# Performance work log

Measured on AMD Instinct MI355X. Metric: run time of the kernel, lower is better.

Reference implementation:

```python
import jax, jax.numpy as jnp
import numpy as np

B, N, D = 8, 1024, 768
H = 12
HD = D // H  # 64
SCALE = HD ** -0.5


def setup_inputs() -> dict:
    key = jax.random.key(0)
    k1, k2, k3 = jax.random.split(key, 3)
    x = jax.random.normal(k1, (B, N, D), dtype=jnp.float32)
    qkv_w = jax.random.normal(k2, (3 * D, D), dtype=jnp.float32) * 0.02
    proj_w = jax.random.normal(k3, (D, D), dtype=jnp.float32) * 0.02
    proj_b = jnp.zeros((D,), dtype=jnp.float32)
    return {"x": x, "qkv_w": qkv_w, "proj_w": proj_w, "proj_b": proj_b}


def reference(x, qkv_w, proj_w, proj_b):
    # qkv projection: [B,N,3D] -> [3,B,H,N,HD]
    qkv = jnp.einsum('bnd,ed->bne', x, qkv_w)
    qkv = qkv.reshape(B, N, 3, H, HD).transpose(2, 0, 3, 1, 4)
    q, k, v = qkv[0], qkv[1], qkv[2]
    # scaled dot-product attention
    attn = jnp.einsum('bhqd,bhkd->bhqk', q * SCALE, k)
    attn = jax.nn.softmax(attn, axis=-1)
    out = jnp.einsum('bhqk,bhkd->bhqd', attn, v)
    out = out.transpose(0, 2, 1, 3).reshape(B, N, D)
    # output projection
    return jnp.einsum('bnd,ed->bne', out, proj_w) + proj_b
```

## Files before the change

### kernel.cpp

```cpp
#include <hip/hip_runtime.h>

typedef unsigned short ushort;
typedef __attribute__((ext_vector_type(4)))  float  f32x4;
typedef __attribute__((ext_vector_type(16))) float  f32x16;
typedef __attribute__((ext_vector_type(8)))  short  s16x8;
typedef __attribute__((ext_vector_type(4)))  ushort u16x4;
typedef __attribute__((ext_vector_type(4)))  unsigned u32x4;

#define MFMA16(a, b, c) __builtin_amdgcn_mfma_f32_16x16x32_bf16((a), (b), (c), 0, 0, 0)
#define MFMA32(a, b, c) __builtin_amdgcn_mfma_f32_32x32x16_bf16((a), (b), (c), 0, 0, 0)

__device__ __forceinline__ ushort f2bf(float f) {
    unsigned u = __builtin_bit_cast(unsigned, f);
    u = (u + 0x7FFF + ((u >> 16) & 1)) >> 16;
    return (ushort)u;
}

__device__ __forceinline__ unsigned cvtpk_bf16(float lo, float hi) {
    unsigned r;
    asm("v_cvt_pk_bf16_f32 %0, %1, %2" : "=v"(r) : "v"(lo), "v"(hi));
    return r;
}
__device__ __forceinline__ void plswap(unsigned& a, unsigned& b) {
    asm volatile("v_permlane32_swap_b32 %0, %1" : "+v"(a), "+v"(b));
}
__device__ __forceinline__ float pairmax(float x) {
    unsigned a = __builtin_bit_cast(unsigned, x), b;
    asm("v_mov_b32 %0, %1" : "=v"(b) : "v"(a));
    plswap(a, b);
    return fmaxf(__builtin_bit_cast(float, a), __builtin_bit_cast(float, b));
}
__device__ __forceinline__ float pairsum(float x) {
    unsigned a = __builtin_bit_cast(unsigned, x), b;
    asm("v_mov_b32 %0, %1" : "=v"(b) : "v"(a));
    plswap(a, b);
    return __builtin_bit_cast(float, a) + __builtin_bit_cast(float, b);
}
__device__ __forceinline__ float fast_exp2(float x) {
    float r;
    asm("v_exp_f32 %0, %1" : "=v"(r) : "v"(x));
    return r;
}

__device__ __forceinline__ void gload_lds16(const ushort* g, ushort* l) {
    __builtin_amdgcn_global_load_lds(
        (const __attribute__((address_space(1))) void*)g,
        (__attribute__((address_space(3))) void*)l, 16, 0, 0);
}

__global__ __launch_bounds__(256) void cvt_all(
    const float* __restrict__ x, const float* __restrict__ wq,
    const float* __restrict__ wp, ushort* __restrict__ out,
    int n4x, int n4q, int n4p)
{
    int i = blockIdx.x * blockDim.x + threadIdx.x;
    const int stride = gridDim.x * blockDim.x;
    const int total = n4x + n4q + n4p;
    for (; i < total; i += stride) {
        float4 v;
        if (i < n4x)            v = ((const float4*)x)[i];
        else if (i < n4x + n4q) v = ((const float4*)wq)[i - n4x];
        else                    v = ((const float4*)wp)[i - n4x - n4q];
        u16x4 o;
        o[0] = f2bf(v.x); o[1] = f2bf(v.y); o[2] = f2bf(v.z); o[3] = f2bf(v.w);
        ((u16x4*)out)[i] = o;
    }
}

__device__ __forceinline__ void gemm128_mainloop(
    const ushort* __restrict__ A, const ushort* __restrict__ B, int K,
    int row0, int col0, ushort* As, ushort* Bs, f32x4 acc[4][4])
{
    const int t  = threadIdx.x;
    const int l  = t & 63;
    const int w  = t >> 6;
    const int lr = l & 15, lg = l >> 4;
    const int wm = w >> 1, wn = w & 1;

#pragma unroll
    for (int m = 0; m < 4; m++)
#pragma unroll
        for (int n = 0; n < 4; n++) acc[m][n] = (f32x4){0.f, 0.f, 0.f, 0.f};

    const int slot = (t & 3) ^ ((t >> 3) & 3);
    const ushort* ga0 = A + (row0 + (t >> 2)) * K + slot * 8;
    const ushort* gb0 = B + (col0 + (t >> 2)) * K + slot * 8;
    const int rowsz = 64 * K;
    ushort* la0 = As + t * 8;
    ushort* lb0 = Bs + t * 8;

    auto STAGE = [&](int kt, int buf) {
        const int k0  = kt * 32;
        const int off = buf * 4096;
        gload_lds16(ga0 + k0,         la0 + off);
        gload_lds16(ga0 + rowsz + k0, la0 + off + 2048);
        gload_lds16(gb0 + k0,         lb0 + off);
        gload_lds16(gb0 + rowsz + k0, lb0 + off + 2048);
    };
    const int sx = (lg ^ ((lr >> 1) & 3)) * 8;
    auto COMPUTE = [&](int buf) {
        const ushort* Ab = As + buf * 4096;
        const ushort* Bb = Bs + buf * 4096;
        s16x8 af[4], bfr[4];
#pragma unroll
        for (int m = 0; m < 4; m++)
            af[m] = *(const s16x8*)&Ab[(wm * 64 + m * 16 + lr) * 32 + sx];
#pragma unroll
        for (int n = 0; n < 4; n++)
            bfr[n] = *(const s16x8*)&Bb[(wn * 64 + n * 16 + lr) * 32 + sx];
        __builtin_amdgcn_s_setprio(1);
#pragma unroll
        for (int m = 0; m < 4; m++)
#pragma unroll
            for (int n = 0; n < 4; n++)
                acc[m][n] = MFMA16(af[m], bfr[n], acc[m][n]);
        __builtin_amdgcn_s_setprio(0);
    };

    const int nt = K >> 5;
    STAGE(0, 0);
    STAGE(1, 1);
    asm volatile("s_waitcnt vmcnt(4)" ::: "memory");
    __builtin_amdgcn_s_barrier();

#define GSTEP(IT, CBUF, SBUF)                                          \
    {                                                                  \
        const int sk = (IT) + 2;                                       \
        const bool st = sk < nt;                                       \
        if (st) STAGE(sk, SBUF);                                       \
        COMPUTE(CBUF);                                                 \
        if (st) { asm volatile("s_waitcnt vmcnt(4)" ::: "memory"); }   \
        else    { asm volatile("s_waitcnt vmcnt(0)" ::: "memory"); }   \
        __builtin_amdgcn_s_barrier();                                  \
    }

    for (int base = 0; base < nt; base += 3) {
        GSTEP(base,     0, 2);
        GSTEP(base + 1, 1, 0);
        GSTEP(base + 2, 2, 1);
    }
#undef GSTEP
}

__global__ __launch_bounds__(256) void qkv_gemm(
    const ushort* __restrict__ X, const ushort* __restrict__ W,
    ushort* __restrict__ qb, ushort* __restrict__ kb, ushort* __restrict__ vb)
{
    __shared__ __align__(16) ushort As[3 * 128 * 32];
    __shared__ __align__(16) ushort Bs[3 * 128 * 32];
    f32x4 acc[4][4];
    const int br = blockIdx.x, bc = blockIdx.y;
    gemm128_mainloop(X, W, 768, br * 128, bc * 128, As, Bs, acc);

    const int t = threadIdx.x, l = t & 63, w = t >> 6;
    const int lr = l & 15, lg = l >> 4, wm = w >> 1, wn = w & 1;
    const int p = (bc * 128) / 768;
    const int mrow0 = br * 128 + wm * 64 + lg * 4;
    const int ecolB = bc * 128 + wn * 64 + lr;
    const float QSCALE = 0.125f * 1.44269504088896f;

#pragma unroll
    for (int n = 0; n < 4; n++) {
        const int e   = ecolB + n * 16;
        const int rem = e - p * 768;
        const int h   = rem >> 6;
        const int hd  = rem & 63;
#pragma unroll
        for (int m = 0; m < 4; m++) {
            const int mr = mrow0 + m * 16;
            const int b  = mr >> 10;
            const int nn = mr & 1023;
            const f32x4 v = acc[m][n];
            const int bh = b * 12 + h;
            if (p == 0) {
                ushort* dst = qb + (bh * 1024 + nn) * 64 + hd;
#pragma unroll
                for (int r = 0; r < 4; r++) dst[r * 64] = f2bf(v[r] * QSCALE);
            } else if (p == 1) {
                ushort* dst = kb + (bh * 1024 + nn) * 64 + hd;
#pragma unroll
                for (int r = 0; r < 4; r++) dst[r * 64] = f2bf(v[r]);
            } else {
                u16x4 pk;
                pk[0] = f2bf(v[0]); pk[1] = f2bf(v[1]);
                pk[2] = f2bf(v[2]); pk[3] = f2bf(v[3]);
                *(u16x4*)(vb + (bh * 64 + hd) * 1024 + nn) = pk;
            }
        }
    }
}

__global__ __launch_bounds__(256) void attn_kernel(
    const ushort* __restrict__ qb, const ushort* __restrict__ kb,
    const ushort* __restrict__ vb, ushort* __restrict__ ao)
{
    __shared__ __align__(16) ushort KV[2][4096];
    const int bh = blockIdx.x, qt = blockIdx.y;
    const int b = bh / 12, h = bh - b * 12;
    const int t = threadIdx.x, l = t & 63, w = t >> 6;
    const int lq = l & 31, hi = l >> 5;
    const int qr0 = qt * 128 + w * 32;

    const int l3 = l >> 3, l7 = l & 7;
    const int ku = w * 8 + l3;
    const int pfv = l7 ^ l3;
    const char* ksrc = (const char*)kb + (size_t)(bh * 1024 + ku) * 128
                     + ((l7 ^ l3) << 4);
    const char* vsrc = (const char*)vb + (size_t)(bh * 64 + ku + 32 * ((pfv >> 2) & 1)) * 2048
                     + ((pfv & 3) << 4);
    ushort* kdst = &KV[0][0]    + w * 512 + l * 8;
    ushort* vdst = &KV[0][2048] + w * 512 + l * 8;

    const ushort* qlane = qb + (bh * 1024 + qr0 + lq) * 64 + hi * 8;
    s16x8 qf[4];
#pragma unroll
    for (int s = 0; s < 4; s++) qf[s] = *(const s16x8*)(qlane + s * 16);

    float m = -__builtin_inff();
    float lsum = 0.f;
    f32x16 o0 = {}, o1 = {};

    gload_lds16((const ushort*)ksrc, kdst);
    gload_lds16((const ushort*)vsrc, vdst);
    __syncthreads();

    const int fx = (lq & 7) << 4;
    for (int it = 0; it < 32; ++it) {
        const int cur = it & 1;
        if (it < 31) {
            const int kvn = (it + 1) * 32;
            gload_lds16((const ushort*)(ksrc + kvn * 128), kdst + (cur ^ 1) * 4096);
            gload_lds16((const ushort*)(vsrc + kvn * 2),   vdst + (cur ^ 1) * 4096);
        }
        const char* Kb = (const char*)&KV[cur][0];
        const char* Vb = (const char*)&KV[cur][2048];

        s16x8 kf[4];
#pragma unroll
        for (int s = 0; s < 4; s++)
            kf[s] = *(const s16x8*)(Kb + lq * 128 + ((hi * 16 + s * 32) ^ fx));

        f32x16 sa = {};
        __builtin_amdgcn_s_setprio(1);
#pragma unroll
        for (int s = 0; s < 4; s++) sa = MFMA32(kf[s], qf[s], sa);
        __builtin_amdgcn_s_setprio(0);

        float g0 = fmaxf(fmaxf(sa[0],  sa[1]),  sa[2]);
        float g1 = fmaxf(fmaxf(sa[3],  sa[4]),  sa[5]);
        float g2 = fmaxf(fmaxf(sa[6],  sa[7]),  sa[8]);
        float g3 = fmaxf(fmaxf(sa[9],  sa[10]), sa[11]);
        float g4 = fmaxf(fmaxf(sa[12], sa[13]), sa[14]);
        float h0 = fmaxf(fmaxf(g0, g1), g2);
        float h1 = fmaxf(fmaxf(g3, g4), sa[15]);
        const float mx = pairmax(fmaxf(h0, h1));

        if (!__all(mx <= m + 8.f)) {
            const float mn = fmaxf(m, mx);
            const float fac = fast_exp2(m - mn);
            m = mn;
            lsum *= fac;
#pragma unroll
            for (int r = 0; r < 16; r++) { o0[r] *= fac; o1[r] *= fac; }
        }

        float p[16];
#pragma unroll
        for (int r = 0; r < 16; r++) p[r] = fast_exp2(sa[r] - m);
        float ts[8];
#pragma unroll
        for (int r = 0; r < 8; r++) ts[r] = p[r] + p[r + 8];
#pragma unroll
        for (int s = 4; s; s >>= 1)
#pragma unroll
            for (int r = 0; r < s; r++) ts[r] += ts[r + s];
        lsum += pairsum(ts[0]);

        s16x8 pfr[2];
#pragma unroll
        for (int slot = 0; slot < 2; slot++) {
            const int r0 = slot * 8;
            unsigned a0 = cvtpk_bf16(p[r0 + 0], p[r0 + 1]);
            unsigned a1 = cvtpk_bf16(p[r0 + 4], p[r0 + 5]);
            plswap(a0, a1);
            unsigned b0 = cvtpk_bf16(p[r0 + 2], p[r0 + 3]);
            unsigned b1 = cvtpk_bf16(p[r0 + 6], p[r0 + 7]);
            plswap(b0, b1);
            const u32x4 u = {a0, b0, a1, b1};
            pfr[slot] = __builtin_bit_cast(s16x8, u);
        }

        s16x8 vf[2][2];
#pragma unroll
        for (int half = 0; half < 2; half++)
#pragma unroll
            for (int s = 0; s < 2; s++)
                vf[half][s] = *(const s16x8*)(Vb + lq * 128 + ((half * 64 + hi * 16 + s * 32) ^ fx));
        __builtin_amdgcn_s_setprio(1);
        o0 = MFMA32(vf[0][0], pfr[0], o0);
        o1 = MFMA32(vf[1][0], pfr[0], o1);
        o0 = MFMA32(vf[0][1], pfr[1], o0);
        o1 = MFMA32(vf[1][1], pfr[1], o1);
        __builtin_amdgcn_s_setprio(0);

        __syncthreads();
    }

    const float inv = 1.f / lsum;
    ushort* op = ao + (b * 1024 + qr0 + lq) * 768 + h * 64 + 4 * hi;
#pragma unroll
    for (int i = 0; i < 4; i++) {
        u16x4 pk0, pk1;
#pragma unroll
        for (int j = 0; j < 4; j++) {
            pk0[j] = f2bf(o0[4 * i + j] * inv);
            pk1[j] = f2bf(o1[4 * i + j] * inv);
        }
        *(u16x4*)(op + 8 * i)      = pk0;
        *(u16x4*)(op + 32 + 8 * i) = pk1;
    }
}

__global__ __launch_bounds__(256) void proj_gemm(
    const ushort* __restrict__ A, const ushort* __restrict__ W,
    const float* __restrict__ bias, float* __restrict__ out)
{
    __shared__ __align__(16) ushort As[3 * 128 * 32];
    __shared__ __align__(16) ushort Bs[3 * 128 * 32];
    f32x4 acc[4][4];
    const int br = blockIdx.x, bc = blockIdx.y;
    gemm128_mainloop(A, W, 768, br * 128, bc * 128, As, Bs, acc);

    const int t = threadIdx.x, l = t & 63, w = t >> 6;
    const int lr = l & 15, lg = l >> 4, wm = w >> 1, wn = w & 1;
    const int mrow0 = br * 128 + wm * 64 + lg * 4;
    const int ecolB = bc * 128 + wn * 64 + lr;

#pragma unroll
    for (int n = 0; n < 4; n++) {
        const int e = ecolB + n * 16;
        const float bv = bias[e];
#pragma unroll
        for (int m = 0; m < 4; m++) {
            const int mr = mrow0 + m * 16;
#pragma unroll
            for (int r = 0; r < 4; r++)
                out[(mr + r) * 768 + e] = acc[m][n][r] + bv;
        }
    }
}

extern "C" void kernel_launch(void* const* d_in, const int* in_sizes, int n_in,
                              void* d_out, int out_size, void* d_ws, size_t ws_size,
                              hipStream_t stream)
{
    const float* x  = (const float*)d_in[0];
    const float* wq = (const float*)d_in[1];
    const float* wp = (const float*)d_in[2];
    const float* pb = (const float*)d_in[3];
    float* out = (float*)d_out;

    const int NX = 8 * 1024 * 768;
    const int NQ = 2304 * 768;
    const int NP = 768 * 768;
    const int SEG = 8 * 12 * 1024 * 64;

    ushort* xb  = (ushort*)d_ws;
    ushort* wqb = xb + NX;
    ushort* wpb = wqb + NQ;
    ushort* qb  = wpb + NP;
    ushort* kb  = qb + SEG;
    ushort* vb  = kb + SEG;
    ushort* ao  = xb;

    cvt_all<<<2048, 256, 0, stream>>>(x, wq, wp, xb, NX / 4, NQ / 4, NP / 4);

    qkv_gemm  <<<dim3(64, 18), 256, 0, stream>>>(xb, wqb, qb, kb, vb);
    attn_kernel<<<dim3(96, 8), 256, 0, stream>>>(qb, kb, vb, ao);
    proj_gemm <<<dim3(64, 6), 256, 0, stream>>>(ao, wpb, pb, out);
}
```

Before: 115.2 us.

## Use 64-key tiles with triple-buffered LDS and MFMA-based row sums in attention

```diff
diff --git a/kernel.cpp b/kernel.cpp
--- a/kernel.cpp
+++ b/kernel.cpp
@@ -29,12 +29,6 @@
     asm("v_mov_b32 %0, %1" : "=v"(b) : "v"(a));
     plswap(a, b);
     return fmaxf(__builtin_bit_cast(float, a), __builtin_bit_cast(float, b));
-}
-__device__ __forceinline__ float pairsum(float x) {
-    unsigned a = __builtin_bit_cast(unsigned, x), b;
-    asm("v_mov_b32 %0, %1" : "=v"(b) : "v"(a));
-    plswap(a, b);
-    return __builtin_bit_cast(float, a) + __builtin_bit_cast(float, b);
 }
 __device__ __forceinline__ float fast_exp2(float x) {
     float r;
@@ -194,119 +188,159 @@
     const ushort* __restrict__ qb, const ushort* __restrict__ kb,
     const ushort* __restrict__ vb, ushort* __restrict__ ao)
 {
-    __shared__ __align__(16) ushort KV[2][4096];
+    __shared__ __align__(16) ushort KV[3][8192];
     const int bh = blockIdx.x, qt = blockIdx.y;
     const int b = bh / 12, h = bh - b * 12;
     const int t = threadIdx.x, l = t & 63, w = t >> 6;
     const int lq = l & 31, hi = l >> 5;
     const int qr0 = qt * 128 + w * 32;
 
-    const int l3 = l >> 3, l7 = l & 7;
-    const int ku = w * 8 + l3;
-    const int pfv = l7 ^ l3;
-    const char* ksrc = (const char*)kb + (size_t)(bh * 1024 + ku) * 128
-                     + ((l7 ^ l3) << 4);
-    const char* vsrc = (const char*)vb + (size_t)(bh * 64 + ku + 32 * ((pfv >> 2) & 1)) * 2048
-                     + ((pfv & 3) << 4);
-    ushort* kdst = &KV[0][0]    + w * 512 + l * 8;
-    ushort* vdst = &KV[0][2048] + w * 512 + l * 8;
+    const int srow = t >> 3;
+    const int ss   = (t & 7) ^ (srow & 7);
+    const ushort* ksrc = kb + (size_t)(bh * 1024 + srow) * 64 + ss * 8;
+    const ushort* vsrc = vb + (size_t)(bh * 64 + srow) * 1024 + ss * 8;
+    ushort* kdst = &KV[0][0]    + t * 8;
+    ushort* vdst = &KV[0][4096] + t * 8;
+
+    auto STAGE = [&](int kt, int buf) {
+        const ushort* ks = ksrc + kt * 4096;
+        const ushort* vs = vsrc + kt * 64;
+        ushort* kd = kdst + buf * 8192;
+        ushort* vd = vdst + buf * 8192;
+        gload_lds16(ks,             kd);
+        gload_lds16(ks + 2048,      kd + 2048);
+        gload_lds16(vs,             vd);
+        gload_lds16(vs + 32 * 1024, vd + 2048);
+    };
 
     const ushort* qlane = qb + (bh * 1024 + qr0 + lq) * 64 + hi * 8;
     s16x8 qf[4];
 #pragma unroll
     for (int s = 0; s < 4; s++) qf[s] = *(const s16x8*)(qlane + s * 16);
 
+    const unsigned one2 = 0x3F803F80u;
+    const u32x4 onev = {one2, one2, one2, one2};
+    const s16x8 onesf = __builtin_bit_cast(s16x8, onev);
+
     float m = -__builtin_inff();
-    float lsum = 0.f;
-    f32x16 o0 = {}, o1 = {};
-
-    gload_lds16((const ushort*)ksrc, kdst);
-    gload_lds16((const ushort*)vsrc, vdst);
-    __syncthreads();
+    f32x16 o0 = {}, o1 = {}, ls = {};
+
+    STAGE(0, 0);
+    STAGE(1, 1);
+    asm volatile("s_waitcnt vmcnt(4)" ::: "memory");
+    __builtin_amdgcn_s_barrier();
 
     const int fx = (lq & 7) << 4;
-    for (int it = 0; it < 32; ++it) {
-        const int cur = it & 1;
-        if (it < 31) {
-            const int kvn = (it + 1) * 32;
-            gload_lds16((const ushort*)(ksrc + kvn * 128), kdst + (cur ^ 1) * 4096);
-            gload_lds16((const ushort*)(vsrc + kvn * 2),   vdst + (cur ^ 1) * 4096);
+    int cur = 0;
+    for (int it = 0; it < 16; ++it) {
+        const bool st = it < 14;
+        if (st) {
+            int sbuf = cur + 2; if (sbuf >= 3) sbuf -= 3;
+            STAGE(it + 2, sbuf);
         }
         const char* Kb = (const char*)&KV[cur][0];
-        const char* Vb = (const char*)&KV[cur][2048];
-
-        s16x8 kf[4];
-#pragma unroll
-        for (int s = 0; s < 4; s++)
-            kf[s] = *(const s16x8*)(Kb + lq * 128 + ((hi * 16 + s * 32) ^ fx));
-
-        f32x16 sa = {};
+        const char* Vb = (const char*)&KV[cur][4096];
+
+        s16x8 kfA[4], kfB[4];
+#pragma unroll
+        for (int s = 0; s < 4; s++) {
+            kfA[s] = *(const s16x8*)(Kb + lq * 128        + ((hi * 16 + s * 32) ^ fx));
+            kfB[s] = *(const s16x8*)(Kb + (32 + lq) * 128 + ((hi * 16 + s * 32) ^ fx));
+        }
+
+        f32x16 sa = {}, sb = {};
         __builtin_amdgcn_s_setprio(1);
 #pragma unroll
-        for (int s = 0; s < 4; s++) sa = MFMA32(kf[s], qf[s], sa);
+        for (int s = 0; s < 4; s++) {
+            sa = MFMA32(kfA[s], qf[s], sa);
+            sb = MFMA32(kfB[s], qf[s], sb);
+        }
         __builtin_amdgcn_s_setprio(0);
 
-        float g0 = fmaxf(fmaxf(sa[0],  sa[1]),  sa[2]);
-        float g1 = fmaxf(fmaxf(sa[3],  sa[4]),  sa[5]);
-        float g2 = fmaxf(fmaxf(sa[6],  sa[7]),  sa[8]);
-        float g3 = fmaxf(fmaxf(sa[9],  sa[10]), sa[11]);
-        float g4 = fmaxf(fmaxf(sa[12], sa[13]), sa[14]);
-        float h0 = fmaxf(fmaxf(g0, g1), g2);
-        float h1 = fmaxf(fmaxf(g3, g4), sa[15]);
-        const float mx = pairmax(fmaxf(h0, h1));
+        float tm[8];
+#pragma unroll
+        for (int r = 0; r < 8; r++)
+            tm[r] = fmaxf(fmaxf(sa[r], sa[r + 8]), fmaxf(sb[r], sb[r + 8]));
+        float u0 = fmaxf(fmaxf(tm[0], tm[1]), fmaxf(tm[2], tm[3]));
+        float u1 = fmaxf(fmaxf(tm[4], tm[5]), fmaxf(tm[6], tm[7]));
+        const float mx = pairmax(fmaxf(u0, u1));
 
         if (!__all(mx <= m + 8.f)) {
             const float mn = fmaxf(m, mx);
             const float fac = fast_exp2(m - mn);
             m = mn;
-            lsum *= fac;
+            ls[0] *= fac;
 #pragma unroll
             for (int r = 0; r < 16; r++) { o0[r] *= fac; o1[r] *= fac; }
         }
 
-        float p[16];
-#pragma unroll
-        for (int r = 0; r < 16; r++) p[r] = fast_exp2(sa[r] - m);
-        float ts[8];
-#pragma unroll
-        for (int r = 0; r < 8; r++) ts[r] = p[r] + p[r + 8];
-#pragma unroll
-        for (int s = 4; s; s >>= 1)
-#pragma unroll
-            for (int r = 0; r < s; r++) ts[r] += ts[r + s];
-        lsum += pairsum(ts[0]);
-
-        s16x8 pfr[2];
-#pragma unroll
-        for (int slot = 0; slot < 2; slot++) {
-            const int r0 = slot * 8;
-            unsigned a0 = cvtpk_bf16(p[r0 + 0], p[r0 + 1]);
-            unsigned a1 = cvtpk_bf16(p[r0 + 4], p[r0 + 5]);
-            plswap(a0, a1);
-            unsigned b0 = cvtpk_bf16(p[r0 + 2], p[r0 + 3]);
-            unsigned b1 = cvtpk_bf16(p[r0 + 6], p[r0 + 7]);
-            plswap(b0, b1);
-            const u32x4 u = {a0, b0, a1, b1};
-            pfr[slot] = __builtin_bit_cast(s16x8, u);
-        }
-
-        s16x8 vf[2][2];
+        s16x8 pfA[2], pfB[2];
+        {
+            float pa[16];
+#pragma unroll
+            for (int r = 0; r < 16; r++) pa[r] = fast_exp2(sa[r] - m);
+#pragma unroll
+            for (int slot = 0; slot < 2; slot++) {
+                const int r0 = slot * 8;
+                unsigned a0 = cvtpk_bf16(pa[r0 + 0], pa[r0 + 1]);
+                unsigned a1 = cvtpk_bf16(pa[r0 + 4], pa[r0 + 5]);
+                plswap(a0, a1);
+                unsigned b0 = cvtpk_bf16(pa[r0 + 2], pa[r0 + 3]);
+                unsigned b1 = cvtpk_bf16(pa[r0 + 6], pa[r0 + 7]);
+                plswap(b0, b1);
+                const u32x4 u = {a0, b0, a1, b1};
+                pfA[slot] = __builtin_bit_cast(s16x8, u);
+            }
+        }
+        {
+            float pb[16];
+#pragma unroll
+            for (int r = 0; r < 16; r++) pb[r] = fast_exp2(sb[r] - m);
+#pragma unroll
+            for (int slot = 0; slot < 2; slot++) {
+                const int r0 = slot * 8;
+                unsigned a0 = cvtpk_bf16(pb[r0 + 0], pb[r0 + 1]);
+                unsigned a1 = cvtpk_bf16(pb[r0 + 4], pb[r0 + 5]);
+                plswap(a0, a1);
+                unsigned b0 = cvtpk_bf16(pb[r0 + 2], pb[r0 + 3]);
+                unsigned b1 = cvtpk_bf16(pb[r0 + 6], pb[r0 + 7]);
+                plswap(b0, b1);
+                const u32x4 u = {a0, b0, a1, b1};
+                pfB[slot] = __builtin_bit_cast(s16x8, u);
+            }
+        }
+
+        s16x8 vA[2][2], vB[2][2];
 #pragma unroll
         for (int half = 0; half < 2; half++)
 #pragma unroll
-            for (int s = 0; s < 2; s++)
-                vf[half][s] = *(const s16x8*)(Vb + lq * 128 + ((half * 64 + hi * 16 + s * 32) ^ fx));
+            for (int s = 0; s < 2; s++) {
+                const int rowb = (32 * half + lq) * 128;
+                vA[half][s] = *(const s16x8*)(Vb + rowb + ((s * 32 + hi * 16) ^ fx));
+                vB[half][s] = *(const s16x8*)(Vb + rowb + ((64 + s * 32 + hi * 16) ^ fx));
+            }
         __builtin_amdgcn_s_setprio(1);
-        o0 = MFMA32(vf[0][0], pfr[0], o0);
-        o1 = MFMA32(vf[1][0], pfr[0], o1);
-        o0 = MFMA32(vf[0][1], pfr[1], o0);
-        o1 = MFMA32(vf[1][1], pfr[1], o1);
+        o0 = MFMA32(vA[0][0], pfA[0], o0);
+        o1 = MFMA32(vA[1][0], pfA[0], o1);
+        o0 = MFMA32(vA[0][1], pfA[1], o0);
+        o1 = MFMA32(vA[1][1], pfA[1], o1);
+        o0 = MFMA32(vB[0][0], pfB[0], o0);
+        o1 = MFMA32(vB[1][0], pfB[0], o1);
+        o0 = MFMA32(vB[0][1], pfB[1], o0);
+        o1 = MFMA32(vB[1][1], pfB[1], o1);
+        ls = MFMA32(onesf, pfA[0], ls);
+        ls = MFMA32(onesf, pfA[1], ls);
+        ls = MFMA32(onesf, pfB[0], ls);
+        ls = MFMA32(onesf, pfB[1], ls);
         __builtin_amdgcn_s_setprio(0);
 
-        __syncthreads();
-    }
-
-    const float inv = 1.f / lsum;
+        if (st) { asm volatile("s_waitcnt vmcnt(4)" ::: "memory"); }
+        else    { asm volatile("s_waitcnt vmcnt(0)" ::: "memory"); }
+        __builtin_amdgcn_s_barrier();
+        cur = (cur == 2) ? 0 : cur + 1;
+    }
+
+    const float inv = 1.f / ls[0];
     ushort* op = ao + (b * 1024 + qr0 + lq) * 768 + h * 64 + 4 * hi;
 #pragma unroll
     for (int i = 0; i < 4; i++) {
```

New measurement: 122.9 us. +6.7%, slower.

## Replace QKV GEMM with 256x256-tile, 512-thread double-buffered kernel

Applied to the files above, without the earlier changes.

```diff
diff --git a/kernel.cpp b/kernel.cpp
--- a/kernel.cpp
+++ b/kernel.cpp
@@ -67,6 +67,152 @@
     }
 }
 
+__global__ __launch_bounds__(512, 2) void qkv_gemm256(
+    const ushort* __restrict__ X, const ushort* __restrict__ W,
+    ushort* __restrict__ qb, ushort* __restrict__ kb, ushort* __restrict__ vb)
+{
+    __shared__ __align__(16) ushort LA[2][16384];
+    __shared__ __align__(16) ushort LB[2][16384];
+
+    const int t  = threadIdx.x;
+    const int l  = t & 63;
+    const int w  = t >> 6;
+    const int lr = l & 15, lg = l >> 4;
+    const int wm = w >> 2, wn = w & 3;
+    const int br = blockIdx.x, bc = blockIdx.y;
+    const int fx = (lr & 7) << 4;
+
+    f32x4 acc[8][4];
+#pragma unroll
+    for (int m = 0; m < 8; m++)
+#pragma unroll
+        for (int n = 0; n < 4; n++) acc[m][n] = (f32x4){0.f, 0.f, 0.f, 0.f};
+
+    const int ss = (t & 7) ^ ((t >> 3) & 7);
+    const ushort* aRow = X + (size_t)(br * 256 + (t >> 3)) * 768 + ss * 8;
+    const ushort* bRow = W + (size_t)(bc * 256 + (t >> 3)) * 768 + ss * 8;
+
+    auto stA_raw = [&](int kt, int h, int buf) {
+        const ushort* s = aRow + (size_t)(h * 128) * 768 + kt * 64;
+        gload_lds16(s,            &LA[buf][h * 8192 + t * 8]);
+        gload_lds16(s + 64 * 768, &LA[buf][h * 8192 + 4096 + t * 8]);
+    };
+    auto stB_raw = [&](int kt, int h, int buf) {
+        const ushort* s = bRow + (size_t)(h * 128) * 768 + kt * 64;
+        gload_lds16(s,            &LB[buf][h * 8192 + t * 8]);
+        gload_lds16(s + 64 * 768, &LB[buf][h * 8192 + 4096 + t * 8]);
+    };
+    auto stA = [&](int kt, int h, int buf) {
+        if ((unsigned)(kt - 2) < 10u) stA_raw(kt, h, buf);
+    };
+    auto stB = [&](int kt, int h, int buf) {
+        if ((unsigned)(kt - 2) < 10u) stB_raw(kt, h, buf);
+    };
+
+    s16x8 fa[4][2], fb0[2][2], fb1[2][2];
+
+#define RD_A(BUF, MI0)                                                       \
+    _Pragma("unroll") for (int i_ = 0; i_ < 4; i_++)                         \
+    _Pragma("unroll") for (int kk = 0; kk < 2; kk++)                         \
+        fa[i_][kk] = *(const s16x8*)((const char*)&LA[BUF][0] +              \
+            (wm * 128 + (MI0 + i_) * 16 + lr) * 128 + ((kk * 64 + lg * 16) ^ fx));
+#define RD_B(BUF, NI0, FB)                                                   \
+    _Pragma("unroll") for (int n_ = 0; n_ < 2; n_++)                         \
+    _Pragma("unroll") for (int kk = 0; kk < 2; kk++)                         \
+        FB[n_][kk] = *(const s16x8*)((const char*)&LB[BUF][0] +              \
+            (wn * 64 + (NI0 + n_) * 16 + lr) * 128 + ((kk * 64 + lg * 16) ^ fx));
+#define MFMA_Q(MI0, NI0, FB)                                                 \
+    __builtin_amdgcn_s_setprio(1);                                           \
+    _Pragma("unroll") for (int i_ = 0; i_ < 4; i_++)                         \
+    _Pragma("unroll") for (int n_ = 0; n_ < 2; n_++)                         \
+    _Pragma("unroll") for (int kk = 0; kk < 2; kk++)                         \
+        acc[MI0 + i_][NI0 + n_] =                                            \
+            MFMA16(fa[i_][kk], FB[n_][kk], acc[MI0 + i_][NI0 + n_]);         \
+    __builtin_amdgcn_s_setprio(0);
+#define BAR() __builtin_amdgcn_s_barrier()
+
+    stA_raw(0, 0, 0); stA_raw(0, 1, 0); stB_raw(0, 0, 0); stB_raw(0, 1, 0);
+    stA_raw(1, 0, 1); stA_raw(1, 1, 1); stB_raw(1, 0, 1); stB_raw(1, 1, 1);
+    asm volatile("s_waitcnt vmcnt(0)" ::: "memory");
+    BAR();
+
+    for (int j = 0; j < 6; ++j) {
+        const int k1 = 2 * j + 1, k2 = 2 * j + 2, k3 = 2 * j + 3;
+        RD_A(0, 0); RD_B(0, 0, fb0);
+        stA(k1, 0, 1);
+        BAR(); MFMA_Q(0, 0, fb0); BAR();
+
+        RD_B(0, 2, fb1);
+        stA(k1, 1, 1);
+        BAR(); MFMA_Q(0, 2, fb1); BAR();
+
+        RD_A(0, 4);
+        stB(k2, 0, 0);
+        BAR(); MFMA_Q(4, 0, fb0); BAR();
+
+        stB(k2, 1, 0);
+        BAR(); MFMA_Q(4, 2, fb1);
+        if (j == 5) { asm volatile("s_waitcnt vmcnt(0)" ::: "memory"); }
+        else        { asm volatile("s_waitcnt vmcnt(4)" ::: "memory"); }
+        BAR();
+
+        RD_A(1, 0); RD_B(1, 0, fb0);
+        stA(k2, 0, 0);
+        BAR(); MFMA_Q(0, 0, fb0); BAR();
+
+        RD_B(1, 2, fb1);
+        stA(k2, 1, 0);
+        BAR(); MFMA_Q(0, 2, fb1); BAR();
+
+        RD_A(1, 4);
+        stB(k3, 0, 1);
+        BAR(); MFMA_Q(4, 0, fb0); BAR();
+
+        stB(k3, 1, 1);
+        BAR(); MFMA_Q(4, 2, fb1);
+        asm volatile("s_waitcnt vmcnt(4)" ::: "memory");
+        BAR();
+    }
+#undef RD_A
+#undef RD_B
+#undef MFMA_Q
+#undef BAR
+
+    const int p = bc / 3;
+    const int mrow0 = br * 256 + wm * 128 + lg * 4;
+    const int ecol0 = (bc - p * 3) * 256 + wn * 64 + lr;
+    const float QSCALE = 0.125f * 1.44269504088896f;
+
+#pragma unroll
+    for (int n = 0; n < 4; n++) {
+        const int rem = ecol0 + n * 16;
+        const int h   = rem >> 6;
+        const int hd  = rem & 63;
+#pragma unroll
+        for (int m = 0; m < 8; m++) {
+            const int mr = mrow0 + m * 16;
+            const int b  = mr >> 10;
+            const int nn = mr & 1023;
+            const f32x4 v = acc[m][n];
+            const int bh = b * 12 + h;
+            if (p == 0) {
+                ushort* dst = qb + (bh * 1024 + nn) * 64 + hd;
+#pragma unroll
+                for (int r = 0; r < 4; r++) dst[r * 64] = f2bf(v[r] * QSCALE);
+            } else if (p == 1) {
+                ushort* dst = kb + (bh * 1024 + nn) * 64 + hd;
+#pragma unroll
+                for (int r = 0; r < 4; r++) dst[r * 64] = f2bf(v[r]);
+            } else {
+                u16x4 pk;
+                pk[0] = f2bf(v[0]); pk[1] = f2bf(v[1]);
+                pk[2] = f2bf(v[2]); pk[3] = f2bf(v[3]);
+                *(u16x4*)(vb + (bh * 64 + hd) * 1024 + nn) = pk;
+            }
+        }
+    }
+}
+
 __device__ __forceinline__ void gemm128_mainloop(
     const ushort* __restrict__ A, const ushort* __restrict__ B, int K,
     int row0, int col0, ushort* As, ushort* Bs, f32x4 acc[4][4])
@@ -140,54 +286,6 @@
         GSTEP(base + 2, 2, 1);
     }
 #undef GSTEP
-}
-
-__global__ __launch_bounds__(256) void qkv_gemm(
-    const ushort* __restrict__ X, const ushort* __restrict__ W,
-    ushort* __restrict__ qb, ushort* __restrict__ kb, ushort* __restrict__ vb)
-{
-    __shared__ __align__(16) ushort As[3 * 128 * 32];
-    __shared__ __align__(16) ushort Bs[3 * 128 * 32];
-    f32x4 acc[4][4];
-    const int br = blockIdx.x, bc = blockIdx.y;
-    gemm128_mainloop(X, W, 768, br * 128, bc * 128, As, Bs, acc);
-
-    const int t = threadIdx.x, l = t & 63, w = t >> 6;
-    const int lr = l & 15, lg = l >> 4, wm = w >> 1, wn = w & 1;
-    const int p = (bc * 128) / 768;
-    const int mrow0 = br * 128 + wm * 64 + lg * 4;
-    const int ecolB = bc * 128 + wn * 64 + lr;
-    const float QSCALE = 0.125f * 1.44269504088896f;
-
-#pragma unroll
-    for (int n = 0; n < 4; n++) {
-        const int e   = ecolB + n * 16;
-        const int rem = e - p * 768;
-        const int h   = rem >> 6;
-        const int hd  = rem & 63;
-#pragma unroll
-        for (int m = 0; m < 4; m++) {
-            const int mr = mrow0 + m * 16;
-            const int b  = mr >> 10;
-            const int nn = mr & 1023;
-            const f32x4 v = acc[m][n];
-            const int bh = b * 12 + h;
-            if (p == 0) {
-                ushort* dst = qb + (bh * 1024 + nn) * 64 + hd;
-#pragma unroll
-                for (int r = 0; r < 4; r++) dst[r * 64] = f2bf(v[r] * QSCALE);
-            } else if (p == 1) {
-                ushort* dst = kb + (bh * 1024 + nn) * 64 + hd;
-#pragma unroll
-                for (int r = 0; r < 4; r++) dst[r * 64] = f2bf(v[r]);
-            } else {
-                u16x4 pk;
-                pk[0] = f2bf(v[0]); pk[1] = f2bf(v[1]);
-                pk[2] = f2bf(v[2]); pk[3] = f2bf(v[3]);
-                *(u16x4*)(vb + (bh * 64 + hd) * 1024 + nn) = pk;
-            }
-        }
-    }
 }
 
 __global__ __launch_bounds__(256) void attn_kernel(
@@ -375,7 +473,7 @@
 
     cvt_all<<<2048, 256, 0, stream>>>(x, wq, wp, xb, NX / 4, NQ / 4, NP / 4);
 
-    qkv_gemm  <<<dim3(64, 18), 256, 0, stream>>>(xb, wqb, qb, kb, vb);
+    qkv_gemm256<<<dim3(32, 9), 512, 0, stream>>>(xb, wqb, qb, kb, vb);
     attn_kernel<<<dim3(96, 8), 256, 0, stream>>>(qb, kb, vb, ao);
     proj_gemm <<<dim3(64, 6), 256, 0, stream>>>(ao, wpb, pb, out);
 }
```

Result: slower. 131.4 us (+14.1%).

## Triple-buffer attention KV loads and retile projection GEMM to 64-row tiles

Applied to the files above, without the earlier changes.

```diff
diff --git a/kernel.cpp b/kernel.cpp
--- a/kernel.cpp
+++ b/kernel.cpp
@@ -194,7 +194,7 @@
     const ushort* __restrict__ qb, const ushort* __restrict__ kb,
     const ushort* __restrict__ vb, ushort* __restrict__ ao)
 {
-    __shared__ __align__(16) ushort KV[2][4096];
+    __shared__ __align__(16) ushort KV[3][4096];
     const int bh = blockIdx.x, qt = blockIdx.y;
     const int b = bh / 12, h = bh - b * 12;
     const int t = threadIdx.x, l = t & 63, w = t >> 6;
@@ -208,8 +208,13 @@
                      + ((l7 ^ l3) << 4);
     const char* vsrc = (const char*)vb + (size_t)(bh * 64 + ku + 32 * ((pfv >> 2) & 1)) * 2048
                      + ((pfv & 3) << 4);
-    ushort* kdst = &KV[0][0]    + w * 512 + l * 8;
-    ushort* vdst = &KV[0][2048] + w * 512 + l * 8;
+    ushort* kdst = &KV[0][0]    + t * 8;
+    ushort* vdst = &KV[0][2048] + t * 8;
+
+    auto STAGE = [&](int kt, int buf) {
+        gload_lds16((const ushort*)(ksrc + kt * 32 * 128), kdst + buf * 4096);
+        gload_lds16((const ushort*)(vsrc + kt * 32 * 2),   vdst + buf * 4096);
+    };
 
     const ushort* qlane = qb + (bh * 1024 + qr0 + lq) * 64 + hi * 8;
     s16x8 qf[4];
@@ -220,17 +225,18 @@
     float lsum = 0.f;
     f32x16 o0 = {}, o1 = {};
 
-    gload_lds16((const ushort*)ksrc, kdst);
-    gload_lds16((const ushort*)vsrc, vdst);
-    __syncthreads();
+    STAGE(0, 0);
+    STAGE(1, 1);
+    asm volatile("s_waitcnt vmcnt(2)" ::: "memory");
+    __builtin_amdgcn_s_barrier();
 
     const int fx = (lq & 7) << 4;
+    int cur = 0;
     for (int it = 0; it < 32; ++it) {
-        const int cur = it & 1;
-        if (it < 31) {
-            const int kvn = (it + 1) * 32;
-            gload_lds16((const ushort*)(ksrc + kvn * 128), kdst + (cur ^ 1) * 4096);
-            gload_lds16((const ushort*)(vsrc + kvn * 2),   vdst + (cur ^ 1) * 4096);
+        const bool st = it < 30;
+        if (st) {
+            int sb = cur + 2; if (sb >= 3) sb -= 3;
+            STAGE(it + 2, sb);
         }
         const char* Kb = (const char*)&KV[cur][0];
         const char* Vb = (const char*)&KV[cur][2048];
@@ -303,7 +309,10 @@
         o1 = MFMA32(vf[1][1], pfr[1], o1);
         __builtin_amdgcn_s_setprio(0);
 
-        __syncthreads();
+        if (st) { asm volatile("s_waitcnt vmcnt(2)" ::: "memory"); }
+        else    { asm volatile("s_waitcnt vmcnt(0)" ::: "memory"); }
+        __builtin_amdgcn_s_barrier();
+        cur = (cur == 2) ? 0 : cur + 1;
     }
 
     const float inv = 1.f / lsum;
@@ -325,23 +334,83 @@
     const ushort* __restrict__ A, const ushort* __restrict__ W,
     const float* __restrict__ bias, float* __restrict__ out)
 {
-    __shared__ __align__(16) ushort As[3 * 128 * 32];
+    __shared__ __align__(16) ushort As[3 * 64 * 32];
     __shared__ __align__(16) ushort Bs[3 * 128 * 32];
-    f32x4 acc[4][4];
+    const int t = threadIdx.x, l = t & 63, w = t >> 6;
+    const int lr = l & 15, lg = l >> 4;
+    const int wm = w >> 1, wn = w & 1;
     const int br = blockIdx.x, bc = blockIdx.y;
-    gemm128_mainloop(A, W, 768, br * 128, bc * 128, As, Bs, acc);
-
-    const int t = threadIdx.x, l = t & 63, w = t >> 6;
-    const int lr = l & 15, lg = l >> 4, wm = w >> 1, wn = w & 1;
-    const int mrow0 = br * 128 + wm * 64 + lg * 4;
+
+    f32x4 acc[2][4];
+#pragma unroll
+    for (int m = 0; m < 2; m++)
+#pragma unroll
+        for (int n = 0; n < 4; n++) acc[m][n] = (f32x4){0.f, 0.f, 0.f, 0.f};
+
+    const int slot = (t & 3) ^ ((t >> 3) & 3);
+    const ushort* ga0 = A + (br * 64 + (t >> 2)) * 768 + slot * 8;
+    const ushort* gb0 = W + (bc * 128 + (t >> 2)) * 768 + slot * 8;
+    ushort* la0 = As + t * 8;
+    ushort* lb0 = Bs + t * 8;
+
+    auto STAGE = [&](int kt, int buf) {
+        const int k0 = kt * 32;
+        gload_lds16(ga0 + k0,            la0 + buf * 2048);
+        gload_lds16(gb0 + k0,            lb0 + buf * 4096);
+        gload_lds16(gb0 + 64 * 768 + k0, lb0 + buf * 4096 + 2048);
+    };
+    const int sx = (lg ^ ((lr >> 1) & 3)) * 8;
+    auto COMPUTE = [&](int buf) {
+        const ushort* Ab = As + buf * 2048;
+        const ushort* Bb = Bs + buf * 4096;
+        s16x8 af[2], bfr[4];
+#pragma unroll
+        for (int m = 0; m < 2; m++)
+            af[m] = *(const s16x8*)&Ab[(wm * 32 + m * 16 + lr) * 32 + sx];
+#pragma unroll
+        for (int n = 0; n < 4; n++)
+            bfr[n] = *(const s16x8*)&Bb[(wn * 64 + n * 16 + lr) * 32 + sx];
+        __builtin_amdgcn_s_setprio(1);
+#pragma unroll
+        for (int m = 0; m < 2; m++)
+#pragma unroll
+            for (int n = 0; n < 4; n++)
+                acc[m][n] = MFMA16(af[m], bfr[n], acc[m][n]);
+        __builtin_amdgcn_s_setprio(0);
+    };
+
+    const int nt = 24;
+    STAGE(0, 0);
+    STAGE(1, 1);
+    asm volatile("s_waitcnt vmcnt(3)" ::: "memory");
+    __builtin_amdgcn_s_barrier();
+
+#define GSTEP(IT, CBUF, SBUF)                                          \
+    {                                                                  \
+        const int sk = (IT) + 2;                                       \
+        const bool st = sk < nt;                                       \
+        if (st) STAGE(sk, SBUF);                                       \
+        COMPUTE(CBUF);                                                 \
+        if (st) { asm volatile("s_waitcnt vmcnt(3)" ::: "memory"); }   \
+        else    { asm volatile("s_waitcnt vmcnt(0)" ::: "memory"); }   \
+        __builtin_amdgcn_s_barrier();                                  \
+    }
+
+    for (int base = 0; base < nt; base += 3) {
+        GSTEP(base,     0, 2);
+        GSTEP(base + 1, 1, 0);
+        GSTEP(base + 2, 2, 1);
+    }
+#undef GSTEP
+
+    const int mrow0 = br * 64 + wm * 32 + lg * 4;
     const int ecolB = bc * 128 + wn * 64 + lr;
-
 #pragma unroll
     for (int n = 0; n < 4; n++) {
         const int e = ecolB + n * 16;
         const float bv = bias[e];
 #pragma unroll
-        for (int m = 0; m < 4; m++) {
+        for (int m = 0; m < 2; m++) {
             const int mr = mrow0 + m * 16;
 #pragma unroll
             for (int r = 0; r < 4; r++)
@@ -377,5 +446,5 @@
 
     qkv_gemm  <<<dim3(64, 18), 256, 0, stream>>>(xb, wqb, qb, kb, vb);
     attn_kernel<<<dim3(96, 8), 256, 0, stream>>>(qb, kb, vb, ao);
-    proj_gemm <<<dim3(64, 6), 256, 0, stream>>>(ao, wpb, pb, out);
-}
+    proj_gemm <<<dim3(128, 6), 256, 0, stream>>>(ao, wpb, pb, out);
+}
```

Result: slower. 119.5 us (+3.7%).
